# Performance work log

Measured on AMD Instinct MI355X. Metric: run time of the kernel, lower is better.

## Reference

```python
import jax, jax.numpy as jnp
import numpy as np

B, T, D = 512, 512, 256          # batch, timesteps, input feature dim
H0, H1, H2, H3 = 32, 64, 64, 64  # VanillaRNN, LSTM, LSTM, GRU hidden sizes
NC = 12                          # num_cumulants


def setup_inputs() -> dict:
    key = jax.random.key(0)
    ks = jax.random.split(key, 12)
    f32 = jnp.float32

    def w(k, shape, fan_in):
        return jax.random.normal(k, shape, f32) * f32(1.0 / np.sqrt(fan_in))

    inp = {}
    inp["pixels_observation"] = jax.random.normal(ks[0], (B, T, D), f32)
    # VanillaRNN(32): input_to_hidden Linear(D->32), hidden_to_hidden Linear(32->32), both with bias
    inp["van_wi"] = w(ks[1], (D, H0), D)
    inp["van_bi"] = jnp.zeros((H0,), f32)
    inp["van_wh"] = w(ks[2], (H0, H0), H0)
    inp["van_bh"] = jnp.zeros((H0,), f32)
    # LSTM(64) on 32-dim input: Linear(32+64 -> 4*64)
    inp["lstm1_w"] = w(ks[3], (H0 + H1, 4 * H1), H0 + H1)
    inp["lstm1_b"] = jnp.zeros((4 * H1,), f32)
    # LSTM(64) on 64-dim input
    inp["lstm2_w"] = w(ks[4], (H1 + H2, 4 * H2), H1 + H2)
    inp["lstm2_b"] = jnp.zeros((4 * H2,), f32)
    # GRU(64)
    inp["gru_wi"] = w(ks[5], (H2, 3 * H3), H2)
    inp["gru_wh"] = w(ks[6], (H3, 3 * H3), H3)
    inp["gru_b"] = jnp.zeros((3 * H3,), f32)
    # MLP (32, 32, 12)
    inp["mlp_w1"] = w(ks[7], (H3, 32), H3)
    inp["mlp_b1"] = jnp.zeros((32,), f32)
    inp["mlp_w2"] = w(ks[8], (32, 32), 32)
    inp["mlp_b2"] = jnp.zeros((32,), f32)
    inp["mlp_w3"] = w(ks[9], (32, NC), 32)
    inp["mlp_b3"] = jnp.zeros((NC,), f32)
    # learned successor_features parameter (preference_vectors = ones(NC,1) constant)
    inp["successor_features"] = jax.random.normal(ks[10], (NC, 1), f32)
    inp["action_index"] = 0
    return inp


def _lstm_step(x, h, c, w, b):
    # haiku LSTM: gates on concat([x, h]); split order i, g, f, o; forget bias +1
    gated = jnp.concatenate([x, h], axis=-1) @ w + b
    i, g, f, o = jnp.split(gated, 4, axis=-1)
    c = jax.nn.sigmoid(f + 1.0) * c + jax.nn.sigmoid(i) * jnp.tanh(g)
    h = jax.nn.sigmoid(o) * jnp.tanh(c)
    return h, c


def reference(pixels_observation, van_wi, van_bi, van_wh, van_bh,
              lstm1_w, lstm1_b, lstm2_w, lstm2_b,
              gru_wi, gru_wh, gru_b,
              mlp_w1, mlp_b1, mlp_w2, mlp_b2, mlp_w3, mlp_b3,
              successor_features, action_index):
    assert action_index == 0  # source selects branch with a static Python int
    x = pixels_observation
    Bsz = x.shape[0]
    f32 = x.dtype

    def step(carry, x_t):
        h0, h1, c1, h2, c2, h3 = carry
        # VanillaRNN: relu(Wi x + bi + Wh h + bh)
        h0 = jax.nn.relu(x_t @ van_wi + van_bi + h0 @ van_wh + van_bh)
        h1, c1 = _lstm_step(h0, h1, c1, lstm1_w, lstm1_b)
        h2, c2 = _lstm_step(h1, h2, c2, lstm2_w, lstm2_b)
        # haiku GRU
        gates_x = h2 @ gru_wi                       # [B, 3H]
        zr_x, a_x = gates_x[:, :2 * H3], gates_x[:, 2 * H3:]
        zr = zr_x + h3 @ gru_wh[:, :2 * H3] + gru_b[:2 * H3]
        z, r = jnp.split(jax.nn.sigmoid(zr), 2, axis=-1)
        a = jnp.tanh(a_x + (r * h3) @ gru_wh[:, 2 * H3:] + gru_b[2 * H3:])
        h3 = (1.0 - z) * h3 + z * a
        return (h0, h1, c1, h2, c2, h3), None

    init = (jnp.zeros((Bsz, H0), f32),
            jnp.zeros((Bsz, H1), f32), jnp.zeros((Bsz, H1), f32),
            jnp.zeros((Bsz, H2), f32), jnp.zeros((Bsz, H2), f32),
            jnp.zeros((Bsz, H3), f32))
    carry, _ = jax.lax.scan(step, init, jnp.swapaxes(x, 0, 1))  # time-major scan
    emb = carry[-1]  # final GRU output = DeepRNN output at last timestep

    # MLP (32, 32, NC): relu on hidden layers, linear final layer
    emb = jax.nn.relu(emb @ mlp_w1 + mlp_b1)
    emb = jax.nn.relu(emb @ mlp_w2 + mlp_b2)
    emb = emb @ mlp_w3 + mlp_b3                     # [B, NC]

    preference_vectors = jnp.ones((NC, 1), f32)
    # einsum('ca,bc->ba', pref * succ, emb)
    policy_params = emb @ (preference_vectors * successor_features)  # [B, 1]
    return successor_features, preference_vectors, policy_params
```

## Files before the change

### kernel.cpp

```cpp
#include <hip/hip_runtime.h>
#include <stdint.h>

#define Tsz 512
#define Dsz 256

#define R_VAN 0
#define R_L1A 1
#define R_L1B 2
#define R_L2A 3
#define R_L2B 4
#define R_GX  5
#define R_GR0 6
#define R_GR1 7

union UHp { uint32_t u; _Float16 s[2]; };
__device__ __forceinline__ uint32_t packh(float a, float b) {
    UHp x; x.s[0] = (_Float16)a; x.s[1] = (_Float16)b; return x.u;
}
__device__ __forceinline__ float dot2(uint32_t w, uint32_t a, float c) {
#if __has_builtin(__builtin_amdgcn_fdot2)
    typedef _Float16 h2 __attribute__((ext_vector_type(2)));
    union U { uint32_t u; h2 h; };
    U W, A; W.u = w; A.u = a;
    return __builtin_amdgcn_fdot2(W.h, A.h, c, false);
#else
    float d;
    asm("v_dot2_f32_f16 %0, %1, %2, %3" : "=v"(d) : "v"(w), "v"(a), "v"(c));
    return d;
#endif
}
__device__ __forceinline__ float fsig(float x)  { return 1.0f / (1.0f + __expf(-x)); }
__device__ __forceinline__ float ftanh(float x) { return 2.0f / (1.0f + __expf(-2.0f * x)) - 1.0f; }

#define D4(ACC, WP, V) \
    do { ACC = dot2((WP)[0], (V).x, ACC); ACC = dot2((WP)[1], (V).y, ACC); \
         ACC = dot2((WP)[2], (V).z, ACC); ACC = dot2((WP)[3], (V).w, ACC); } while (0)
#define D4X(A, X, WP, V) \
    do { A = dot2((WP)[0], (V).x, A); X = dot2((WP)[1], (V).y, X); \
         A = dot2((WP)[2], (V).z, A); X = dot2((WP)[3], (V).w, X); } while (0)

#define WAITGE(cache, ridx, need) \
    do { if ((cache) < (need)) { \
        volatile const int* _pf = (volatile const int*)&prog[(ridx)]; \
        int _v = *_pf; \
        while (_v < (need)) _v = *_pf; \
        (cache) = _v; } } while (0)

#define SIGNAL(ridx, val) \
    do { asm volatile("s_waitcnt lgkmcnt(0)" ::: "memory"); \
         *((volatile int*)&prog[(ridx)]) = (val); } while (0)

__global__ __launch_bounds__(512, 1) void rnn_flag(
    const float* __restrict__ pix,
    const float* __restrict__ van_wi, const float* __restrict__ van_bi,
    const float* __restrict__ van_wh, const float* __restrict__ van_bh,
    const float* __restrict__ w1g, const float* __restrict__ b1g,
    const float* __restrict__ w2g, const float* __restrict__ b2g,
    const float* __restrict__ gwi, const float* __restrict__ gwh,
    const float* __restrict__ gb,
    const float* __restrict__ mw1, const float* __restrict__ mb1,
    const float* __restrict__ mw2, const float* __restrict__ mb2,
    const float* __restrict__ mw3, const float* __restrict__ mb3,
    const float* __restrict__ sf,
    float* __restrict__ out)
{
    const int tid  = threadIdx.x;
    const int wv   = tid >> 6;
    const int lane = tid & 63;
    const int r0   = 2 * blockIdx.x;

    int role;
    switch (wv) {
        case 0: role = R_L2A; break;
        case 1: role = R_L2B; break;
        case 2: role = R_VAN; break;
        case 3: role = R_GX;  break;
        case 4: role = R_GR0; break;
        case 5: role = R_GR1; break;
        case 6: role = R_L1A; break;
        default: role = R_L1B; break;
    }

    __shared__ __align__(16) _Float16 xb [4][2][256];
    __shared__ __align__(16) _Float16 h0b[4][2][32];
    __shared__ __align__(16) _Float16 h1b[4][2][64];
    __shared__ __align__(16) _Float16 h2b[4][2][64];
    __shared__ __align__(16) _Float16 gxb[4][2][192];
    __shared__ __align__(16) _Float16 h3s[2][64];
    __shared__ __align__(16) _Float16 rh3s[2][64];
    __shared__ int prog[8];
    __shared__ float sHf[2][64];
    __shared__ float sT[2][64];
    __shared__ float sP[2][12];

    uint32_t wreg[128];
    float bz0 = 0.f, bz1 = 0.f, bz2 = 0.f;
    float st0 = 0.f, st1 = 0.f;
    float4 pxA0{}, pxB0{}, pxA1{}, pxB1{};
    const float* pr0 = nullptr; const float* pr1 = nullptr;

    if (role == R_VAN) {
        const int c = lane & 31, s = lane >> 5;
#pragma unroll
        for (int j = 0; j < 64; ++j)
            wreg[j] = packh(van_wi[(128 * s + 2 * j) * 32 + c],
                            van_wi[(128 * s + 2 * j + 1) * 32 + c]);
#pragma unroll
        for (int j = 0; j < 8; ++j)
            wreg[64 + j] = packh(van_wh[(16 * s + 2 * j) * 32 + c],
                                 van_wh[(16 * s + 2 * j + 1) * 32 + c]);
        bz0 = van_bi[c] + van_bh[c];
        pr0 = pix + (size_t)r0 * Tsz * Dsz;
        pr1 = pr0 + (size_t)Tsz * Dsz;
#pragma unroll
        for (int t = 0; t < 2; ++t) {
            float4 p0 = *(const float4*)(pr0 + (size_t)t * Dsz + 4 * lane);
            float4 p1 = *(const float4*)(pr1 + (size_t)t * Dsz + 4 * lane);
            uint32_t* x0 = (uint32_t*)xb[t][0];
            uint32_t* x1 = (uint32_t*)xb[t][1];
            x0[2 * lane] = packh(p0.x, p0.y); x0[2 * lane + 1] = packh(p0.z, p0.w);
            x1[2 * lane] = packh(p1.x, p1.y); x1[2 * lane + 1] = packh(p1.z, p1.w);
        }
        pxA0 = *(const float4*)(pr0 + 2 * (size_t)Dsz + 4 * lane);
        pxA1 = *(const float4*)(pr1 + 2 * (size_t)Dsz + 4 * lane);
        pxB0 = *(const float4*)(pr0 + 3 * (size_t)Dsz + 4 * lane);
        pxB1 = *(const float4*)(pr1 + 3 * (size_t)Dsz + 4 * lane);
    } else if (role == R_L1A || role == R_L1B) {
        const int p = (role == R_L1A ? 0 : 64) + lane;
        const int u = p >> 1, odd = p & 1;
        const int c0 = odd ? 128 + u : u, c1 = c0 + 64;
#pragma unroll
        for (int j = 0; j < 48; ++j)
            wreg[j] = packh(w1g[(2 * j) * 256 + c0], w1g[(2 * j + 1) * 256 + c0]);
#pragma unroll
        for (int j = 0; j < 48; ++j)
            wreg[48 + j] = packh(w1g[(2 * j) * 256 + c1], w1g[(2 * j + 1) * 256 + c1]);
        bz0 = b1g[c0]; bz1 = b1g[c1];
    } else if (role == R_L2A || role == R_L2B) {
        const int p = (role == R_L2A ? 0 : 64) + lane;
        const int u = p >> 1, odd = p & 1;
        const int c0 = odd ? 128 + u : u, c1 = c0 + 64;
#pragma unroll
        for (int j = 0; j < 64; ++j)
            wreg[j] = packh(w2g[(2 * j) * 256 + c0], w2g[(2 * j + 1) * 256 + c0]);
#pragma unroll
        for (int j = 0; j < 64; ++j)
            wreg[64 + j] = packh(w2g[(2 * j) * 256 + c1], w2g[(2 * j + 1) * 256 + c1]);
        bz0 = b2g[c0]; bz1 = b2g[c1];
    } else if (role == R_GX) {
#pragma unroll
        for (int j = 0; j < 32; ++j) {
            wreg[j]      = packh(gwi[(2 * j) * 192 + lane],       gwi[(2 * j + 1) * 192 + lane]);
            wreg[32 + j] = packh(gwi[(2 * j) * 192 + 64 + lane],  gwi[(2 * j + 1) * 192 + 64 + lane]);
            wreg[64 + j] = packh(gwi[(2 * j) * 192 + 128 + lane], gwi[(2 * j + 1) * 192 + 128 + lane]);
        }
        bz0 = gb[lane]; bz1 = gb[64 + lane]; bz2 = gb[128 + lane];
    } else {
#pragma unroll
        for (int j = 0; j < 32; ++j) {
            wreg[j]      = packh(gwh[(2 * j) * 192 + lane],       gwh[(2 * j + 1) * 192 + lane]);
            wreg[32 + j] = packh(gwh[(2 * j) * 192 + 64 + lane],  gwh[(2 * j + 1) * 192 + 64 + lane]);
            wreg[64 + j] = packh(gwh[(2 * j) * 192 + 128 + lane], gwh[(2 * j + 1) * 192 + 128 + lane]);
        }
    }

    for (int i = tid; i < 4 * 2 * 32;  i += 512) ((_Float16*)h0b)[i] = (_Float16)0.f;
    for (int i = tid; i < 4 * 2 * 64;  i += 512) ((_Float16*)h1b)[i] = (_Float16)0.f;
    for (int i = tid; i < 4 * 2 * 64;  i += 512) ((_Float16*)h2b)[i] = (_Float16)0.f;
    for (int i = tid; i < 4 * 2 * 192; i += 512) ((_Float16*)gxb)[i] = (_Float16)0.f;
    for (int i = tid; i < 2 * 64; i += 512) { ((_Float16*)h3s)[i] = (_Float16)0.f; ((_Float16*)rh3s)[i] = (_Float16)0.f; }
    if (tid < 8) prog[tid] = 0;
    __syncthreads();

    if (role == R_VAN) {
        const int c = lane & 31, s = lane >> 5;
        int cA = 0, cB = 0;
        for (int t = 0; t < Tsz; ++t) {
            WAITGE(cA, R_L1A, t - 3);
            WAITGE(cB, R_L1B, t - 3);
            if (t + 2 < Tsz) {
                uint32_t* x0 = (uint32_t*)xb[(t + 2) & 3][0];
                uint32_t* x1 = (uint32_t*)xb[(t + 2) & 3][1];
                x0[2 * lane] = packh(pxA0.x, pxA0.y); x0[2 * lane + 1] = packh(pxA0.z, pxA0.w);
                x1[2 * lane] = packh(pxA1.x, pxA1.y); x1[2 * lane + 1] = packh(pxA1.z, pxA1.w);
            }
            pxA0 = pxB0; pxA1 = pxB1;
            if (t + 4 < Tsz) {
                pxB0 = *(const float4*)(pr0 + (size_t)(t + 4) * Dsz + 4 * lane);
                pxB1 = *(const float4*)(pr1 + (size_t)(t + 4) * Dsz + 4 * lane);
            }
#pragma unroll
            for (int r = 0; r < 2; ++r) {
                const uint4* xq = ((const uint4*)xb[t & 3][r]) + 16 * s;
                const uint4* hq = ((const uint4*)h0b[(t - 1) & 3][r]) + 2 * s;
                float a0 = 0.f, a1 = 0.f;
#pragma unroll
                for (int q = 0; q < 16; q += 2) {
                    uint4 v0 = xq[q], v1 = xq[q + 1];
                    D4(a0, &wreg[4 * q], v0);
                    D4(a1, &wreg[4 * q + 4], v1);
                }
                {
                    uint4 v0 = hq[0], v1 = hq[1];
                    D4(a0, &wreg[64], v0);
                    D4(a1, &wreg[68], v1);
                }
                float acc = a0 + a1;
                acc += __shfl_xor(acc, 32);
                if (s == 0) h0b[t & 3][r][c] = (_Float16)fmaxf(acc + bz0, 0.f);
            }
            SIGNAL(R_VAN, t + 1);
        }
    } else if (role == R_L1A || role == R_L1B) {
        const int prt = (role == R_L1A) ? R_L1B : R_L1A;
        const int p = (role == R_L1A ? 0 : 64) + lane;
        const int u = p >> 1, odd = p & 1;
        int cv = 0, cp = 0, c2a = 0, c2b = 0;
        for (int t = 0; t < Tsz; ++t) {
            WAITGE(cv, R_VAN, t + 1);
            WAITGE(cp, prt, t);
            WAITGE(c2a, R_L2A, t - 3);
            WAITGE(c2b, R_L2B, t - 3);
#pragma unroll
            for (int r = 0; r < 2; ++r) {
                const uint4* aq = (const uint4*)h0b[t & 3][r];
                const uint4* bq = (const uint4*)h1b[(t - 1) & 3][r];
                float a0 = bz0, a1 = bz1, x0 = 0.f, x1 = 0.f;
#pragma unroll
                for (int q = 0; q < 4; ++q) {
                    uint4 v = aq[q];
                    D4X(a0, x0, &wreg[4 * q], v);
                    D4X(a1, x1, &wreg[48 + 4 * q], v);
                }
#pragma unroll
                for (int q = 0; q < 8; ++q) {
                    uint4 v = bq[q];
                    D4X(a0, x0, &wreg[16 + 4 * q], v);
                    D4X(a1, x1, &wreg[64 + 4 * q], v);
                }
                float g0 = a0 + x0, g1 = a1 + x1;
                float send = 0.f, fq = 0.f, op = 0.f;
                if (!odd) send = fsig(g0) * ftanh(g1);
                else { fq = fsig(g0 + 1.f); op = fsig(g1); }
                float prx = __shfl_xor(send, 1);
                if (odd) {
                    float cs = r ? st1 : st0;
                    cs = fq * cs + prx;
                    if (r) st1 = cs; else st0 = cs;
                    h1b[t & 3][r][u] = (_Float16)(op * ftanh(cs));
                }
            }
            SIGNAL(role, t + 1);
        }
    } else if (role == R_L2A || role == R_L2B) {
        const int prt = (role == R_L2A) ? R_L2B : R_L2A;
        const int p = (role == R_L2A ? 0 : 64) + lane;
        const int u = p >> 1, odd = p & 1;
        int c1a = 0, c1b = 0, cp = 0, cg = 0;
        for (int t = 0; t < Tsz; ++t) {
            WAITGE(c1a, R_L1A, t + 1);
            WAITGE(c1b, R_L1B, t + 1);
            WAITGE(cp, prt, t);
            WAITGE(cg, R_GX, t - 3);
#pragma unroll
            for (int r = 0; r < 2; ++r) {
                const uint4* aq = (const uint4*)h1b[t & 3][r];
                const uint4* bq = (const uint4*)h2b[(t - 1) & 3][r];
                float a0 = bz0, a1 = bz1, x0 = 0.f, x1 = 0.f;
#pragma unroll
                for (int q = 0; q < 8; ++q) {
                    uint4 v = aq[q];
                    D4X(a0, x0, &wreg[4 * q], v);
                    D4X(a1, x1, &wreg[64 + 4 * q], v);
                }
#pragma unroll
                for (int q = 0; q < 8; ++q) {
                    uint4 v = bq[q];
                    D4X(a0, x0, &wreg[32 + 4 * q], v);
                    D4X(a1, x1, &wreg[96 + 4 * q], v);
                }
                float g0 = a0 + x0, g1 = a1 + x1;
                float send = 0.f, fq = 0.f, op = 0.f;
                if (!odd) send = fsig(g0) * ftanh(g1);
                else { fq = fsig(g0 + 1.f); op = fsig(g1); }
                float prx = __shfl_xor(send, 1);
                if (odd) {
                    float cs = r ? st1 : st0;
                    cs = fq * cs + prx;
                    if (r) st1 = cs; else st0 = cs;
                    h2b[t & 3][r][u] = (_Float16)(op * ftanh(cs));
                }
            }
            SIGNAL(role, t + 1);
        }
    } else if (role == R_GX) {
        int c2a = 0, c2b = 0, g0c = 0, g1c = 0;
        for (int t = 0; t < Tsz; ++t) {
            WAITGE(c2a, R_L2A, t + 1);
            WAITGE(c2b, R_L2B, t + 1);
            WAITGE(g0c, R_GR0, t - 3);
            WAITGE(g1c, R_GR1, t - 3);
#pragma unroll
            for (int r = 0; r < 2; ++r) {
                const uint4* hq = (const uint4*)h2b[t & 3][r];
                float az = bz0, ar = bz1, aa = bz2;
#pragma unroll
                for (int q = 0; q < 8; ++q) {
                    uint4 v = hq[q];
                    D4(az, &wreg[4 * q], v);
                    D4(ar, &wreg[32 + 4 * q], v);
                    D4(aa, &wreg[64 + 4 * q], v);
                }
                gxb[t & 3][r][lane]       = (_Float16)az;
                gxb[t & 3][r][64 + lane]  = (_Float16)ar;
                gxb[t & 3][r][128 + lane] = (_Float16)aa;
            }
            SIGNAL(R_GX, t + 1);
        }
    } else {
        const int r = (role == R_GR0) ? 0 : 1;
        int cg = 0;
        for (int t = 0; t < Tsz; ++t) {
            WAITGE(cg, R_GX, t + 1);
            const uint4* hq = (const uint4*)h3s[r];
            float az = (float)gxb[t & 3][r][lane];
            float ar = (float)gxb[t & 3][r][64 + lane];
#pragma unroll
            for (int q = 0; q < 8; ++q) {
                uint4 v = hq[q];
                D4(az, &wreg[4 * q], v);
                D4(ar, &wreg[32 + 4 * q], v);
            }
            float z = fsig(az);
            rh3s[r][lane] = (_Float16)(fsig(ar) * st0);
            float ga = (float)gxb[t & 3][r][128 + lane];
            asm volatile("s_waitcnt lgkmcnt(0)" ::: "memory");
            const uint4* rq = (const uint4*)rh3s[r];
            float aa = ga, ab = 0.f;
#pragma unroll
            for (int q = 0; q < 8; ++q) {
                uint4 v = rq[q];
                if (q & 1) { D4(ab, &wreg[64 + 4 * q], v); }
                else       { D4(aa, &wreg[64 + 4 * q], v); }
            }
            float av = ftanh(aa + ab);
            st0 = (1.f - z) * st0 + z * av;
            h3s[r][lane] = (_Float16)st0;
            SIGNAL(role, t + 1);
        }
    }

    if (role == R_GR0) sHf[0][lane] = st0;
    if (role == R_GR1) sHf[1][lane] = st0;
    __syncthreads();

    if (tid < 64) {
        const int r = tid >> 5, c = tid & 31;
        float acc = mb1[c];
#pragma unroll
        for (int kk = 0; kk < 64; ++kk) acc = fmaf(sHf[r][kk], mw1[kk * 32 + c], acc);
        sT[r][c] = fmaxf(acc, 0.f);
    }
    __syncthreads();
    if (tid < 64) {
        const int r = tid >> 5, c = tid & 31;
        float acc = mb2[c];
#pragma unroll
        for (int kk = 0; kk < 32; ++kk) acc = fmaf(sT[r][kk], mw2[kk * 32 + c], acc);
        sT[r][32 + c] = fmaxf(acc, 0.f);
    }
    __syncthreads();
    if (tid < 24) {
        const int r = tid / 12, c = tid - 12 * r;
        float acc = mb3[c];
#pragma unroll
        for (int kk = 0; kk < 32; ++kk) acc = fmaf(sT[r][32 + kk], mw3[kk * 12 + c], acc);
        sP[r][c] = acc;
    }
    __syncthreads();
    if (tid < 2) {
        float acc = 0.f;
#pragma unroll
        for (int kk = 0; kk < 12; ++kk) acc = fmaf(sP[tid][kk], sf[kk], acc);
        out[24 + r0 + tid] = acc;
    }
    if (blockIdx.x == 0 && tid < 12) {
        out[tid] = sf[tid];
        out[12 + tid] = 1.0f;
    }
}

extern "C" void kernel_launch(void* const* d_in, const int* in_sizes, int n_in,
                              void* d_out, int out_size, void* d_ws, size_t ws_size,
                              hipStream_t stream) {
    (void)in_sizes; (void)n_in; (void)d_ws; (void)ws_size; (void)out_size;
    const float* pix    = (const float*)d_in[0];
    const float* van_wi = (const float*)d_in[1];
    const float* van_bi = (const float*)d_in[2];
    const float* van_wh = (const float*)d_in[3];
    const float* van_bh = (const float*)d_in[4];
    const float* w1     = (const float*)d_in[5];
    const float* b1     = (const float*)d_in[6];
    const float* w2     = (const float*)d_in[7];
    const float* b2     = (const float*)d_in[8];
    const float* gwi    = (const float*)d_in[9];
    const float* gwh    = (const float*)d_in[10];
    const float* gb     = (const float*)d_in[11];
    const float* mw1    = (const float*)d_in[12];
    const float* mb1    = (const float*)d_in[13];
    const float* mw2    = (const float*)d_in[14];
    const float* mb2    = (const float*)d_in[15];
    const float* mw3    = (const float*)d_in[16];
    const float* mb3    = (const float*)d_in[17];
    const float* sf     = (const float*)d_in[18];
    float* out = (float*)d_out;

    rnn_flag<<<256, 512, 0, stream>>>(
        pix, van_wi, van_bi, van_wh, van_bh,
        w1, b1, w2, b2, gwi, gwh, gb,
        mw1, mb1, mw2, mb2, mw3, mb3, sf, out);
}
```

Before: 781.1 us.

## Split RNN pipeline across 16 wavefronts with dedicated loader waves

Doubles the block to 1024 threads and re-partitions the wavefront-specialized recurrent pipeline. LSTM layers now use 4 waves each, with one gate column per lane and shuffles for the cell update. The GRU input projection is split over 3 waves, and two dedicated waves stream pixel rows into shared memory. This shortens each wave's per-step critical path and moves global loads off the vanilla-RNN wave. The cost is more flag waits per step and higher cross-wave synchronization traffic in LDS.

```diff
diff --git a/kernel.cpp b/kernel.cpp
--- a/kernel.cpp
+++ b/kernel.cpp
@@ -4,14 +4,14 @@
 #define Tsz 512
 #define Dsz 256
 
-#define R_VAN 0
-#define R_L1A 1
-#define R_L1B 2
-#define R_L2A 3
-#define R_L2B 4
-#define R_GX  5
-#define R_GR0 6
-#define R_GR1 7
+#define R_STG0 0
+#define R_STG1 1
+#define R_VAN  2
+#define R_L1(w) (3 + (w))
+#define R_L2(w) (7 + (w))
+#define R_GX(w) (11 + (w))
+#define R_GR0 14
+#define R_GR1 15
 
 union UHp { uint32_t u; _Float16 s[2]; };
 __device__ __forceinline__ uint32_t packh(float a, float b) {
@@ -48,9 +48,9 @@
 
 #define SIGNAL(ridx, val) \
     do { asm volatile("s_waitcnt lgkmcnt(0)" ::: "memory"); \
-         *((volatile int*)&prog[(ridx)]) = (val); } while (0)
-
-__global__ __launch_bounds__(512, 1) void rnn_flag(
+         if (lane == 0) *((volatile int*)&prog[(ridx)]) = (val); } while (0)
+
+__global__ __launch_bounds__(1024, 1) void rnn16(
     const float* __restrict__ pix,
     const float* __restrict__ van_wi, const float* __restrict__ van_bi,
     const float* __restrict__ van_wh, const float* __restrict__ van_bh,
@@ -69,18 +69,6 @@
     const int lane = tid & 63;
     const int r0   = 2 * blockIdx.x;
 
-    int role;
-    switch (wv) {
-        case 0: role = R_L2A; break;
-        case 1: role = R_L2B; break;
-        case 2: role = R_VAN; break;
-        case 3: role = R_GX;  break;
-        case 4: role = R_GR0; break;
-        case 5: role = R_GR1; break;
-        case 6: role = R_L1A; break;
-        default: role = R_L1B; break;
-    }
-
     __shared__ __align__(16) _Float16 xb [4][2][256];
     __shared__ __align__(16) _Float16 h0b[4][2][32];
     __shared__ __align__(16) _Float16 h1b[4][2][64];
@@ -88,111 +76,85 @@
     __shared__ __align__(16) _Float16 gxb[4][2][192];
     __shared__ __align__(16) _Float16 h3s[2][64];
     __shared__ __align__(16) _Float16 rh3s[2][64];
-    __shared__ int prog[8];
+    __shared__ int prog[16];
     __shared__ float sHf[2][64];
     __shared__ float sT[2][64];
     __shared__ float sP[2][12];
 
-    uint32_t wreg[128];
-    float bz0 = 0.f, bz1 = 0.f, bz2 = 0.f;
-    float st0 = 0.f, st1 = 0.f;
-    float4 pxA0{}, pxB0{}, pxA1{}, pxB1{};
-    const float* pr0 = nullptr; const float* pr1 = nullptr;
-
-    if (role == R_VAN) {
-        const int c = lane & 31, s = lane >> 5;
+    int kind, wpar;
+    switch (wv) {
+        case 0:  kind = 3; wpar = 0; break;
+        case 4:  kind = 3; wpar = 1; break;
+        case 1:  kind = 3; wpar = 2; break;
+        case 5:  kind = 3; wpar = 3; break;
+        case 2:  kind = 2; wpar = 0; break;
+        case 6:  kind = 2; wpar = 1; break;
+        case 3:  kind = 2; wpar = 2; break;
+        case 7:  kind = 2; wpar = 3; break;
+        case 8:  kind = 5; wpar = 0; break;
+        case 9:  kind = 5; wpar = 1; break;
+        case 10: kind = 4; wpar = 0; break;
+        case 14: kind = 4; wpar = 1; break;
+        case 11: kind = 4; wpar = 2; break;
+        case 12: kind = 0; wpar = 0; break;
+        case 13: kind = 0; wpar = 1; break;
+        default: kind = 1; wpar = 0; break;
+    }
+
+    for (int i = tid; i < 4 * 2 * 32;  i += 1024) ((_Float16*)h0b)[i] = (_Float16)0.f;
+    for (int i = tid; i < 4 * 2 * 64;  i += 1024) ((_Float16*)h1b)[i] = (_Float16)0.f;
+    for (int i = tid; i < 4 * 2 * 64;  i += 1024) ((_Float16*)h2b)[i] = (_Float16)0.f;
+    for (int i = tid; i < 4 * 2 * 192; i += 1024) ((_Float16*)gxb)[i] = (_Float16)0.f;
+    for (int i = tid; i < 2 * 64; i += 1024) { ((_Float16*)h3s)[i] = (_Float16)0.f; ((_Float16*)rh3s)[i] = (_Float16)0.f; }
+    if (tid < 16) prog[tid] = 0;
+
+    float gr_st = 0.f;
+
+    if (kind == 0) {
+        const int r = wpar;
+        const float* pr = pix + (size_t)(r0 + r) * Tsz * Dsz;
+        float4 q0 = *(const float4*)(pr + 0 * (size_t)Dsz + 4 * lane);
+        float4 q1 = *(const float4*)(pr + 1 * (size_t)Dsz + 4 * lane);
+        float4 q2 = *(const float4*)(pr + 2 * (size_t)Dsz + 4 * lane);
+        float4 q3 = *(const float4*)(pr + 3 * (size_t)Dsz + 4 * lane);
+        __syncthreads();
+        int cv = 0;
+        for (int tb = 0; tb < Tsz; tb += 4) {
+#define XSTEP(P, I) do { \
+            const int t = tb + (I); \
+            WAITGE(cv, R_VAN, t - 3); \
+            uint32_t* xw = (uint32_t*)xb[t & 3][r]; \
+            xw[2 * lane]     = packh(P.x, P.y); \
+            xw[2 * lane + 1] = packh(P.z, P.w); \
+            SIGNAL(R_STG0 + r, t + 1); \
+            if (t + 4 < Tsz) P = *(const float4*)(pr + (size_t)(t + 4) * Dsz + 4 * lane); \
+        } while (0)
+            XSTEP(q0, 0); XSTEP(q1, 1); XSTEP(q2, 2); XSTEP(q3, 3);
+#undef XSTEP
+        }
+    } else if (kind == 1) {
+        const int c = lane & 31, sp = lane >> 5;
+        uint32_t wreg[72];
 #pragma unroll
         for (int j = 0; j < 64; ++j)
-            wreg[j] = packh(van_wi[(128 * s + 2 * j) * 32 + c],
-                            van_wi[(128 * s + 2 * j + 1) * 32 + c]);
+            wreg[j] = packh(van_wi[(128 * sp + 2 * j) * 32 + c],
+                            van_wi[(128 * sp + 2 * j + 1) * 32 + c]);
 #pragma unroll
         for (int j = 0; j < 8; ++j)
-            wreg[64 + j] = packh(van_wh[(16 * s + 2 * j) * 32 + c],
-                                 van_wh[(16 * s + 2 * j + 1) * 32 + c]);
-        bz0 = van_bi[c] + van_bh[c];
-        pr0 = pix + (size_t)r0 * Tsz * Dsz;
-        pr1 = pr0 + (size_t)Tsz * Dsz;
-#pragma unroll
-        for (int t = 0; t < 2; ++t) {
-            float4 p0 = *(const float4*)(pr0 + (size_t)t * Dsz + 4 * lane);
-            float4 p1 = *(const float4*)(pr1 + (size_t)t * Dsz + 4 * lane);
-            uint32_t* x0 = (uint32_t*)xb[t][0];
-            uint32_t* x1 = (uint32_t*)xb[t][1];
-            x0[2 * lane] = packh(p0.x, p0.y); x0[2 * lane + 1] = packh(p0.z, p0.w);
-            x1[2 * lane] = packh(p1.x, p1.y); x1[2 * lane + 1] = packh(p1.z, p1.w);
-        }
-        pxA0 = *(const float4*)(pr0 + 2 * (size_t)Dsz + 4 * lane);
-        pxA1 = *(const float4*)(pr1 + 2 * (size_t)Dsz + 4 * lane);
-        pxB0 = *(const float4*)(pr0 + 3 * (size_t)Dsz + 4 * lane);
-        pxB1 = *(const float4*)(pr1 + 3 * (size_t)Dsz + 4 * lane);
-    } else if (role == R_L1A || role == R_L1B) {
-        const int p = (role == R_L1A ? 0 : 64) + lane;
-        const int u = p >> 1, odd = p & 1;
-        const int c0 = odd ? 128 + u : u, c1 = c0 + 64;
-#pragma unroll
-        for (int j = 0; j < 48; ++j)
-            wreg[j] = packh(w1g[(2 * j) * 256 + c0], w1g[(2 * j + 1) * 256 + c0]);
-#pragma unroll
-        for (int j = 0; j < 48; ++j)
-            wreg[48 + j] = packh(w1g[(2 * j) * 256 + c1], w1g[(2 * j + 1) * 256 + c1]);
-        bz0 = b1g[c0]; bz1 = b1g[c1];
-    } else if (role == R_L2A || role == R_L2B) {
-        const int p = (role == R_L2A ? 0 : 64) + lane;
-        const int u = p >> 1, odd = p & 1;
-        const int c0 = odd ? 128 + u : u, c1 = c0 + 64;
-#pragma unroll
-        for (int j = 0; j < 64; ++j)
-            wreg[j] = packh(w2g[(2 * j) * 256 + c0], w2g[(2 * j + 1) * 256 + c0]);
-#pragma unroll
-        for (int j = 0; j < 64; ++j)
-            wreg[64 + j] = packh(w2g[(2 * j) * 256 + c1], w2g[(2 * j + 1) * 256 + c1]);
-        bz0 = b2g[c0]; bz1 = b2g[c1];
-    } else if (role == R_GX) {
-#pragma unroll
-        for (int j = 0; j < 32; ++j) {
-            wreg[j]      = packh(gwi[(2 * j) * 192 + lane],       gwi[(2 * j + 1) * 192 + lane]);
-            wreg[32 + j] = packh(gwi[(2 * j) * 192 + 64 + lane],  gwi[(2 * j + 1) * 192 + 64 + lane]);
-            wreg[64 + j] = packh(gwi[(2 * j) * 192 + 128 + lane], gwi[(2 * j + 1) * 192 + 128 + lane]);
-        }
-        bz0 = gb[lane]; bz1 = gb[64 + lane]; bz2 = gb[128 + lane];
-    } else {
-#pragma unroll
-        for (int j = 0; j < 32; ++j) {
-            wreg[j]      = packh(gwh[(2 * j) * 192 + lane],       gwh[(2 * j + 1) * 192 + lane]);
-            wreg[32 + j] = packh(gwh[(2 * j) * 192 + 64 + lane],  gwh[(2 * j + 1) * 192 + 64 + lane]);
-            wreg[64 + j] = packh(gwh[(2 * j) * 192 + 128 + lane], gwh[(2 * j + 1) * 192 + 128 + lane]);
-        }
-    }
-
-    for (int i = tid; i < 4 * 2 * 32;  i += 512) ((_Float16*)h0b)[i] = (_Float16)0.f;
-    for (int i = tid; i < 4 * 2 * 64;  i += 512) ((_Float16*)h1b)[i] = (_Float16)0.f;
-    for (int i = tid; i < 4 * 2 * 64;  i += 512) ((_Float16*)h2b)[i] = (_Float16)0.f;
-    for (int i = tid; i < 4 * 2 * 192; i += 512) ((_Float16*)gxb)[i] = (_Float16)0.f;
-    for (int i = tid; i < 2 * 64; i += 512) { ((_Float16*)h3s)[i] = (_Float16)0.f; ((_Float16*)rh3s)[i] = (_Float16)0.f; }
-    if (tid < 8) prog[tid] = 0;
-    __syncthreads();
-
-    if (role == R_VAN) {
-        const int c = lane & 31, s = lane >> 5;
-        int cA = 0, cB = 0;
+            wreg[64 + j] = packh(van_wh[(16 * sp + 2 * j) * 32 + c],
+                                 van_wh[(16 * sp + 2 * j + 1) * 32 + c]);
+        const float bz = van_bi[c] + van_bh[c];
+        __syncthreads();
+        int cg0 = 0, cg1 = 0, cl[4] = {0, 0, 0, 0};
         for (int t = 0; t < Tsz; ++t) {
-            WAITGE(cA, R_L1A, t - 3);
-            WAITGE(cB, R_L1B, t - 3);
-            if (t + 2 < Tsz) {
-                uint32_t* x0 = (uint32_t*)xb[(t + 2) & 3][0];
-                uint32_t* x1 = (uint32_t*)xb[(t + 2) & 3][1];
-                x0[2 * lane] = packh(pxA0.x, pxA0.y); x0[2 * lane + 1] = packh(pxA0.z, pxA0.w);
-                x1[2 * lane] = packh(pxA1.x, pxA1.y); x1[2 * lane + 1] = packh(pxA1.z, pxA1.w);
-            }
-            pxA0 = pxB0; pxA1 = pxB1;
-            if (t + 4 < Tsz) {
-                pxB0 = *(const float4*)(pr0 + (size_t)(t + 4) * Dsz + 4 * lane);
-                pxB1 = *(const float4*)(pr1 + (size_t)(t + 4) * Dsz + 4 * lane);
-            }
+            WAITGE(cg0, R_STG0, t + 1);
+            WAITGE(cg1, R_STG1, t + 1);
+#pragma unroll
+            for (int s = 0; s < 4; ++s) WAITGE(cl[s], R_L1(s), t - 3);
 #pragma unroll
             for (int r = 0; r < 2; ++r) {
-                const uint4* xq = ((const uint4*)xb[t & 3][r]) + 16 * s;
-                const uint4* hq = ((const uint4*)h0b[(t - 1) & 3][r]) + 2 * s;
+                const uint4* xq = ((const uint4*)xb[t & 3][r]) + 16 * sp;
+                const uint4* hq = ((const uint4*)h0b[(t - 1) & 3][r]) + 2 * sp;
                 float a0 = 0.f, a1 = 0.f;
 #pragma unroll
                 for (int q = 0; q < 16; q += 2) {
@@ -207,121 +169,143 @@
                 }
                 float acc = a0 + a1;
                 acc += __shfl_xor(acc, 32);
-                if (s == 0) h0b[t & 3][r][c] = (_Float16)fmaxf(acc + bz0, 0.f);
+                if (sp == 0) h0b[t & 3][r][c] = (_Float16)fmaxf(acc + bz, 0.f);
             }
             SIGNAL(R_VAN, t + 1);
         }
-    } else if (role == R_L1A || role == R_L1B) {
-        const int prt = (role == R_L1A) ? R_L1B : R_L1A;
-        const int p = (role == R_L1A ? 0 : 64) + lane;
-        const int u = p >> 1, odd = p & 1;
-        int cv = 0, cp = 0, c2a = 0, c2b = 0;
+    } else if (kind == 2) {
+        const int w = wpar;
+        const int gate = lane >> 4, uo = lane & 15;
+        const int col = gate * 64 + 16 * w + uo;
+        uint32_t wreg[48];
+#pragma unroll
+        for (int j = 0; j < 48; ++j)
+            wreg[j] = packh(w1g[(2 * j) * 256 + col], w1g[(2 * j + 1) * 256 + col]);
+        const float bz = b1g[col];
+        __syncthreads();
+        float cs0 = 0.f, cs1 = 0.f;
+        int cv = 0, csb[3] = {0, 0, 0}, cl2[4] = {0, 0, 0, 0};
         for (int t = 0; t < Tsz; ++t) {
             WAITGE(cv, R_VAN, t + 1);
-            WAITGE(cp, prt, t);
-            WAITGE(c2a, R_L2A, t - 3);
-            WAITGE(c2b, R_L2B, t - 3);
+#pragma unroll
+            for (int s = 1; s < 4; ++s) WAITGE(csb[s - 1], R_L1((w + s) & 3), t);
+#pragma unroll
+            for (int s = 0; s < 4; ++s) WAITGE(cl2[s], R_L2(s), t - 3);
 #pragma unroll
             for (int r = 0; r < 2; ++r) {
                 const uint4* aq = (const uint4*)h0b[t & 3][r];
                 const uint4* bq = (const uint4*)h1b[(t - 1) & 3][r];
-                float a0 = bz0, a1 = bz1, x0 = 0.f, x1 = 0.f;
-#pragma unroll
-                for (int q = 0; q < 4; ++q) {
-                    uint4 v = aq[q];
-                    D4X(a0, x0, &wreg[4 * q], v);
-                    D4X(a1, x1, &wreg[48 + 4 * q], v);
-                }
-#pragma unroll
-                for (int q = 0; q < 8; ++q) {
-                    uint4 v = bq[q];
-                    D4X(a0, x0, &wreg[16 + 4 * q], v);
-                    D4X(a1, x1, &wreg[64 + 4 * q], v);
-                }
-                float g0 = a0 + x0, g1 = a1 + x1;
-                float send = 0.f, fq = 0.f, op = 0.f;
-                if (!odd) send = fsig(g0) * ftanh(g1);
-                else { fq = fsig(g0 + 1.f); op = fsig(g1); }
-                float prx = __shfl_xor(send, 1);
-                if (odd) {
-                    float cs = r ? st1 : st0;
-                    cs = fq * cs + prx;
-                    if (r) st1 = cs; else st0 = cs;
-                    h1b[t & 3][r][u] = (_Float16)(op * ftanh(cs));
-                }
-            }
-            SIGNAL(role, t + 1);
-        }
-    } else if (role == R_L2A || role == R_L2B) {
-        const int prt = (role == R_L2A) ? R_L2B : R_L2A;
-        const int p = (role == R_L2A ? 0 : 64) + lane;
-        const int u = p >> 1, odd = p & 1;
-        int c1a = 0, c1b = 0, cp = 0, cg = 0;
+                float a0 = bz, x0 = 0.f;
+#pragma unroll
+                for (int q = 0; q < 4; ++q) { uint4 v = aq[q]; D4X(a0, x0, &wreg[4 * q], v); }
+#pragma unroll
+                for (int q = 0; q < 8; ++q) { uint4 v = bq[q]; D4X(a0, x0, &wreg[16 + 4 * q], v); }
+                float acc = a0 + x0;
+                float tv;
+                if (gate == 0)      tv = fsig(acc);
+                else if (gate == 1) tv = ftanh(acc);
+                else if (gate == 2) tv = fsig(acc + 1.f);
+                else                tv = fsig(acc);
+                float x16   = __shfl_xor(tv, 16);
+                float prod  = tv * x16;
+                float prodx = __shfl_xor(prod, 32);
+                float cprev = r ? cs1 : cs0;
+                float cnew  = tv * cprev + prodx;
+                if (gate == 2) { if (r) cs1 = cnew; else cs0 = cnew; }
+                float tc  = ftanh(cnew);
+                float tcx = __shfl_xor(tc, 16);
+                if (gate == 3)
+                    h1b[t & 3][r][16 * w + uo] = (_Float16)(tv * tcx);
+            }
+            SIGNAL(R_L1(w), t + 1);
+        }
+    } else if (kind == 3) {
+        const int w = wpar;
+        const int gate = lane >> 4, uo = lane & 15;
+        const int col = gate * 64 + 16 * w + uo;
+        uint32_t wreg[64];
+#pragma unroll
+        for (int j = 0; j < 64; ++j)
+            wreg[j] = packh(w2g[(2 * j) * 256 + col], w2g[(2 * j + 1) * 256 + col]);
+        const float bz = b2g[col];
+        __syncthreads();
+        float cs0 = 0.f, cs1 = 0.f;
+        int cl1[4] = {0, 0, 0, 0}, csb[3] = {0, 0, 0}, cgx[3] = {0, 0, 0};
         for (int t = 0; t < Tsz; ++t) {
-            WAITGE(c1a, R_L1A, t + 1);
-            WAITGE(c1b, R_L1B, t + 1);
-            WAITGE(cp, prt, t);
-            WAITGE(cg, R_GX, t - 3);
+#pragma unroll
+            for (int s = 0; s < 4; ++s) WAITGE(cl1[s], R_L1(s), t + 1);
+#pragma unroll
+            for (int s = 1; s < 4; ++s) WAITGE(csb[s - 1], R_L2((w + s) & 3), t);
+#pragma unroll
+            for (int s = 0; s < 3; ++s) WAITGE(cgx[s], R_GX(s), t - 3);
 #pragma unroll
             for (int r = 0; r < 2; ++r) {
                 const uint4* aq = (const uint4*)h1b[t & 3][r];
                 const uint4* bq = (const uint4*)h2b[(t - 1) & 3][r];
-                float a0 = bz0, a1 = bz1, x0 = 0.f, x1 = 0.f;
-#pragma unroll
-                for (int q = 0; q < 8; ++q) {
-                    uint4 v = aq[q];
-                    D4X(a0, x0, &wreg[4 * q], v);
-                    D4X(a1, x1, &wreg[64 + 4 * q], v);
-                }
-#pragma unroll
-                for (int q = 0; q < 8; ++q) {
-                    uint4 v = bq[q];
-                    D4X(a0, x0, &wreg[32 + 4 * q], v);
-                    D4X(a1, x1, &wreg[96 + 4 * q], v);
-                }
-                float g0 = a0 + x0, g1 = a1 + x1;
-                float send = 0.f, fq = 0.f, op = 0.f;
-                if (!odd) send = fsig(g0) * ftanh(g1);
-                else { fq = fsig(g0 + 1.f); op = fsig(g1); }
-                float prx = __shfl_xor(send, 1);
-                if (odd) {
-                    float cs = r ? st1 : st0;
-                    cs = fq * cs + prx;
-                    if (r) st1 = cs; else st0 = cs;
-                    h2b[t & 3][r][u] = (_Float16)(op * ftanh(cs));
-                }
-            }
-            SIGNAL(role, t + 1);
-        }
-    } else if (role == R_GX) {
-        int c2a = 0, c2b = 0, g0c = 0, g1c = 0;
+                float a0 = bz, x0 = 0.f;
+#pragma unroll
+                for (int q = 0; q < 8; ++q) { uint4 v = aq[q]; D4X(a0, x0, &wreg[4 * q], v); }
+#pragma unroll
+                for (int q = 0; q < 8; ++q) { uint4 v = bq[q]; D4X(a0, x0, &wreg[32 + 4 * q], v); }
+                float acc = a0 + x0;
+                float tv;
+                if (gate == 0)      tv = fsig(acc);
+                else if (gate == 1) tv = ftanh(acc);
+                else if (gate == 2) tv = fsig(acc + 1.f);
+                else                tv = fsig(acc);
+                float x16   = __shfl_xor(tv, 16);
+                float prod  = tv * x16;
+                float prodx = __shfl_xor(prod, 32);
+                float cprev = r ? cs1 : cs0;
+                float cnew  = tv * cprev + prodx;
+                if (gate == 2) { if (r) cs1 = cnew; else cs0 = cnew; }
+                float tc  = ftanh(cnew);
+                float tcx = __shfl_xor(tc, 16);
+                if (gate == 3)
+                    h2b[t & 3][r][16 * w + uo] = (_Float16)(tv * tcx);
+            }
+            SIGNAL(R_L2(w), t + 1);
+        }
+    } else if (kind == 4) {
+        const int w = wpar;
+        const int col = 64 * w + lane;
+        uint32_t wreg[32];
+#pragma unroll
+        for (int j = 0; j < 32; ++j)
+            wreg[j] = packh(gwi[(2 * j) * 192 + col], gwi[(2 * j + 1) * 192 + col]);
+        const float bz = gb[col];
+        __syncthreads();
+        int cl2[4] = {0, 0, 0, 0}, cgr0 = 0, cgr1 = 0;
         for (int t = 0; t < Tsz; ++t) {
-            WAITGE(c2a, R_L2A, t + 1);
-            WAITGE(c2b, R_L2B, t + 1);
-            WAITGE(g0c, R_GR0, t - 3);
-            WAITGE(g1c, R_GR1, t - 3);
+#pragma unroll
+            for (int s = 0; s < 4; ++s) WAITGE(cl2[s], R_L2(s), t + 1);
+            WAITGE(cgr0, R_GR0, t - 3);
+            WAITGE(cgr1, R_GR1, t - 3);
 #pragma unroll
             for (int r = 0; r < 2; ++r) {
                 const uint4* hq = (const uint4*)h2b[t & 3][r];
-                float az = bz0, ar = bz1, aa = bz2;
-#pragma unroll
-                for (int q = 0; q < 8; ++q) {
-                    uint4 v = hq[q];
-                    D4(az, &wreg[4 * q], v);
-                    D4(ar, &wreg[32 + 4 * q], v);
-                    D4(aa, &wreg[64 + 4 * q], v);
-                }
-                gxb[t & 3][r][lane]       = (_Float16)az;
-                gxb[t & 3][r][64 + lane]  = (_Float16)ar;
-                gxb[t & 3][r][128 + lane] = (_Float16)aa;
-            }
-            SIGNAL(R_GX, t + 1);
+                float a0 = bz, x0 = 0.f;
+#pragma unroll
+                for (int q = 0; q < 8; ++q) { uint4 v = hq[q]; D4X(a0, x0, &wreg[4 * q], v); }
+                gxb[t & 3][r][col] = (_Float16)(a0 + x0);
+            }
+            SIGNAL(R_GX(w), t + 1);
         }
     } else {
-        const int r = (role == R_GR0) ? 0 : 1;
-        int cg = 0;
+        const int r = wpar;
+        uint32_t wreg[96];
+#pragma unroll
+        for (int j = 0; j < 32; ++j) {
+            wreg[j]      = packh(gwh[(2 * j) * 192 + lane],       gwh[(2 * j + 1) * 192 + lane]);
+            wreg[32 + j] = packh(gwh[(2 * j) * 192 + 64 + lane],  gwh[(2 * j + 1) * 192 + 64 + lane]);
+            wreg[64 + j] = packh(gwh[(2 * j) * 192 + 128 + lane], gwh[(2 * j + 1) * 192 + 128 + lane]);
+        }
+        __syncthreads();
+        int cg0 = 0, cg1 = 0, cg2 = 0;
         for (int t = 0; t < Tsz; ++t) {
-            WAITGE(cg, R_GX, t + 1);
+            WAITGE(cg0, R_GX(0), t + 1);
+            WAITGE(cg1, R_GX(1), t + 1);
+            WAITGE(cg2, R_GX(2), t + 1);
             const uint4* hq = (const uint4*)h3s[r];
             float az = (float)gxb[t & 3][r][lane];
             float ar = (float)gxb[t & 3][r][64 + lane];
@@ -332,7 +316,7 @@
                 D4(ar, &wreg[32 + 4 * q], v);
             }
             float z = fsig(az);
-            rh3s[r][lane] = (_Float16)(fsig(ar) * st0);
+            rh3s[r][lane] = (_Float16)(fsig(ar) * gr_st);
             float ga = (float)gxb[t & 3][r][128 + lane];
             asm volatile("s_waitcnt lgkmcnt(0)" ::: "memory");
             const uint4* rq = (const uint4*)rh3s[r];
@@ -344,14 +328,14 @@
                 else       { D4(aa, &wreg[64 + 4 * q], v); }
             }
             float av = ftanh(aa + ab);
-            st0 = (1.f - z) * st0 + z * av;
-            h3s[r][lane] = (_Float16)st0;
-            SIGNAL(role, t + 1);
-        }
-    }
-
-    if (role == R_GR0) sHf[0][lane] = st0;
-    if (role == R_GR1) sHf[1][lane] = st0;
+            gr_st = (1.f - z) * gr_st + z * av;
+            h3s[r][lane] = (_Float16)gr_st;
+            SIGNAL(R_GR0 + r, t + 1);
+        }
+    }
+
+    if (wv == 8) sHf[0][lane] = gr_st;
+    if (wv == 9) sHf[1][lane] = gr_st;
     __syncthreads();
 
     if (tid < 64) {
@@ -415,7 +399,7 @@
     const float* sf     = (const float*)d_in[18];
     float* out = (float*)d_out;
 
-    rnn_flag<<<256, 512, 0, stream>>>(
+    rnn16<<<256, 1024, 0, stream>>>(
         pix, van_wi, van_bi, van_wh, van_bh,
         w1, b1, w2, b2, gwi, gwh, gb,
         mw1, mb1, mw2, mb2, mw3, mb3, sf, out);
```

New measurement: 1.147 ms. +46.9%, slower.
